# Kernel optimization log

Measured on AMD Instinct MI355X. Metric: run time of the kernel, lower is better.

Reference implementation:

```python
import jax, jax.numpy as jnp
import numpy as np

B, L, H2, P, A, T = 2048, 128, 600, 50, 50, 3  # batch, seq, 2*hidden, pos_emb, attn, latent types


def setup_inputs() -> dict:
    key = jax.random.key(0)
    ks = jax.random.split(key, 9)
    return {
        "hidden": jax.random.normal(ks[0], (B, L, H2), dtype=jnp.float32),
        "pos1_emb": jax.random.normal(ks[1], (B, L, P), dtype=jnp.float32),
        "pos2_emb": jax.random.normal(ks[2], (B, L, P), dtype=jnp.float32),
        "entity1_idx": jax.random.randint(ks[3], (B,), 0, L),
        "entity2_idx": jax.random.randint(ks[4], (B,), 0, L),
        "W_hid": jax.random.normal(ks[5], (A, H2 + 2 * P), dtype=jnp.float32) * 0.05,
        "W_ent": jax.random.normal(ks[6], (A, 4 * H2), dtype=jnp.float32) * 0.05,
        "latent_types": jax.random.normal(ks[7], (T, H2), dtype=jnp.float32) * 0.05,
        "v": jax.random.normal(ks[8], (A, 1), dtype=jnp.float32) * 0.05,
    }


def _latent_type(ent, latent_types):
    # ent: [B, 1, H2]; latent_types: [T, H2]
    a = jax.nn.softmax(jnp.einsum("bed,td->bet", ent, latent_types), axis=-1)
    return jnp.einsum("bet,td->bed", a, latent_types)  # [B, 1, H2]


def reference(hidden, pos1_emb, pos2_emb, entity1_idx, entity2_idx, W_hid, W_ent, latent_types, v):
    b = hidden.shape[0]
    batch_ix = jnp.arange(b)
    hid_e1 = hidden[batch_ix, entity1_idx][:, None, :]  # [B, 1, H2]
    hid_e2 = hidden[batch_ix, entity2_idx][:, None, :]
    e1_type = _latent_type(hid_e1, latent_types)
    e2_type = _latent_type(hid_e2, latent_types)
    # u1: per-token projection, u2: per-sentence entity projection (broadcast over L)
    u1 = jnp.einsum("bld,ad->bla", jnp.concatenate([hidden, pos1_emb, pos2_emb], axis=-1), W_hid)
    u2 = jnp.einsum("bed,ad->bea", jnp.concatenate([hid_e1, e1_type, hid_e2, e2_type], axis=-1), W_ent)
    u = jnp.tanh(u1 + u2)  # [B, L, A]
    scores = jnp.einsum("bla,a->bl", u, v[:, 0])  # [B, L]
    alpha = jax.nn.softmax(scores, axis=-1)
    z = jnp.einsum("bl,bld->bd", alpha, hidden)  # [B, H2]
    return z
```

## Files before the change

kernel.cpp:

```cpp
#include <hip/hip_runtime.h>
#include <hip/hip_bf16.h>
#include <math.h>


#define B_    2048
#define L_    128
#define H2_   600
#define P_    50
#define A_    50
#define D700  700
#define KCN   22
#define KHALF 11
#define AP    64
#define MT    32
#define XP    712
#define NB    8

typedef __attribute__((ext_vector_type(8))) short short8;
typedef __attribute__((ext_vector_type(4))) float f32x4;

__device__ __forceinline__ unsigned short f2bf(float f) {
  unsigned u = __float_as_uint(f);
  u += 0x7fffu + ((u >> 16) & 1u);
  return (unsigned short)(u >> 16);
}
__device__ __forceinline__ unsigned cvtpk(float a, float b) {
  unsigned r;
  asm("v_cvt_pk_bf16_f32 %0, %1, %2" : "=v"(r) : "v"(a), "v"(b));
  return r;
}
__device__ __forceinline__ float bf2f(unsigned short s) {
  return __uint_as_float(((unsigned)s) << 16);
}

__global__ __launch_bounds__(512, 4) void ku2(const float* __restrict__ hidden,
                                              const int* __restrict__ e1,
                                              const int* __restrict__ e2,
                                              const float* __restrict__ Went,
                                              const float* __restrict__ lt,
                                              const float* __restrict__ Wh,
                                              unsigned short* __restrict__ Wt,
                                              float* __restrict__ u2ws) {
  __shared__ __align__(16) float E[NB][2400];
  __shared__ float dots[NB][2][3];
  __shared__ float aw[NB][2][3];
  int tid = threadIdx.x;
  int b0 = blockIdx.x * NB;

  {
    int gidx = blockIdx.x * 512 + tid;
    if (gidx < KCN * 2048) {
      int kc = gidx >> 11, r = gidx & 2047, a = r >> 5, kk = r & 31;
      int d = kc * 32 + kk;
      float v = (a < A_ && d < D700) ? Wh[a * D700 + d] : 0.f;
      Wt[gidx] = f2bf(v);
    }
  }

  for (int idx = tid; idx < NB * 2 * 150; idx += 512) {
    int i = idx / 300, r = idx - i * 300, e = r / 150, g = r - e * 150;
    int bb = b0 + i;
    int l = e ? e2[bb] : e1[bb];
    float4 f = *(const float4*)(hidden + ((size_t)bb * L_ + l) * H2_ + g * 4);
    *(float4*)(&E[i][e * 1200 + g * 4]) = f;
  }
  __syncthreads();

  int w = tid >> 6, lane = tid & 63;
  #pragma unroll
  for (int j = 0; j < 6; ++j) {
    int i = w, e = (j >= 3) ? 1 : 0, t = j % 3;
    float p = 0.f;
    for (int d = lane; d < 600; d += 64) p += E[i][e * 1200 + d] * lt[t * 600 + d];
    #pragma unroll
    for (int mask = 1; mask <= 32; mask <<= 1) p += __shfl_xor(p, mask);
    if (lane == 0) dots[i][e][t] = p;
  }
  __syncthreads();
  if (tid < NB * 6) {
    int t = tid % 3, e = (tid / 3) & 1, i = tid / 6;
    float d0 = dots[i][e][0], d1 = dots[i][e][1], d2 = dots[i][e][2];
    float m = fmaxf(d0, fmaxf(d1, d2));
    float x0 = expf(d0 - m), x1 = expf(d1 - m), x2 = expf(d2 - m);
    float Z = x0 + x1 + x2;
    aw[i][e][t] = ((t == 0) ? x0 : (t == 1) ? x1 : x2) / Z;
  }
  __syncthreads();
  for (int idx = tid; idx < NB * 2 * 600; idx += 512) {
    int i = idx / 1200, r = idx - i * 1200, e = r / 600, d = r - e * 600;
    float v = aw[i][e][0] * lt[d] + aw[i][e][1] * lt[600 + d] + aw[i][e][2] * lt[1200 + d];
    E[i][e * 1200 + 600 + d] = v;
  }
  __syncthreads();
  for (int a = w; a < A_; a += 8) {
    float acc[NB] = {0.f, 0.f, 0.f, 0.f, 0.f, 0.f, 0.f, 0.f};
    for (int d0 = lane * 4; d0 < 2400; d0 += 256) {
      float4 wv = *(const float4*)(Went + a * 2400 + d0);
      #pragma unroll
      for (int i = 0; i < NB; ++i) {
        float4 ev = *(const float4*)(&E[i][d0]);
        acc[i] += ev.x * wv.x + ev.y * wv.y + ev.z * wv.z + ev.w * wv.w;
      }
    }
    #pragma unroll
    for (int i = 0; i < NB; ++i) {
      float p = acc[i];
      #pragma unroll
      for (int mask = 1; mask <= 32; mask <<= 1) p += __shfl_xor(p, mask);
      if (lane == 0) u2ws[(b0 + i) * AP + a] = p;
    }
  }
  for (int idx = tid; idx < NB * (AP - A_); idx += 512) {
    u2ws[(b0 + idx / (AP - A_)) * AP + A_ + idx % (AP - A_)] = 0.f;
  }
}

__global__ __launch_bounds__(512, 4) void kmain(
    const float* __restrict__ hidden, const float* __restrict__ pos1,
    const float* __restrict__ pos2, const float* __restrict__ vvec,
    const unsigned short* __restrict__ Wt, const float* __restrict__ u2ws,
    float* __restrict__ zp_ws, float* __restrict__ mS_ws) {
  __shared__ __align__(16) unsigned short Xs[MT * XP];
  __shared__ __align__(16) float pacc[4][64][8];
  __shared__ float scores4[4][MT];
  __shared__ float es_s[MT];
  __shared__ float u2s[AP];
  __shared__ float vs[AP];

  int tid = threadIdx.x;
  int T = blockIdx.x;
  int b = T >> 2, tok0 = (T & 3) * MT;
  int w = tid >> 6, lane = tid & 63;
  int acol = lane & 15, kgrp = lane >> 4;

  int t = tid >> 4, c0 = tid & 15;
  const float* rowp = hidden + ((size_t)(b * L_ + tok0) + t) * H2_;
  float4 f[9];
  #pragma unroll
  for (int j = 0; j < 9; ++j) f[j] = *(const float4*)(rowp + (c0 + 16 * j) * 4);
  bool h10 = (c0 < 6);
  float4 f9;
  if (h10) f9 = *(const float4*)(rowp + (c0 + 144) * 4);

  const float* p1 = pos1 + (size_t)(b * L_ + tok0) * P_;
  const float* p2 = pos2 + (size_t)(b * L_ + tok0) * P_;
  float2 q1a = *(const float2*)(p1 + tid * 2);
  float2 q2a = *(const float2*)(p2 + tid * 2);
  bool hq = (tid < 288);
  float2 q1b, q2b;
  if (hq) {
    q1b = *(const float2*)(p1 + (tid + 512) * 2);
    q2b = *(const float2*)(p2 + (tid + 512) * 2);
  }
  float u2v = 0.f, vvv = 0.f;
  if (tid < AP) {
    u2v = u2ws[b * AP + tid];
    vvv = (tid < A_) ? vvec[tid] : 0.f;
  }

  #pragma unroll
  for (int j = 0; j < 9; ++j) {
    uint2 wv2; wv2.x = cvtpk(f[j].x, f[j].y); wv2.y = cvtpk(f[j].z, f[j].w);
    *(uint2*)(&Xs[t * XP + (c0 + 16 * j) * 4]) = wv2;
  }
  if (h10) {
    uint2 wv2; wv2.x = cvtpk(f9.x, f9.y); wv2.y = cvtpk(f9.z, f9.w);
    *(uint2*)(&Xs[t * XP + (c0 + 144) * 4]) = wv2;
  }
  {
    int t1 = tid / 25, g = tid - t1 * 25;
    *(unsigned*)(&Xs[t1 * XP + 600 + g * 2]) = cvtpk(q1a.x, q1a.y);
    *(unsigned*)(&Xs[t1 * XP + 650 + g * 2]) = cvtpk(q2a.x, q2a.y);
  }
  if (hq) {
    int idx = tid + 512;
    int t1 = idx / 25, g = idx - t1 * 25;
    *(unsigned*)(&Xs[t1 * XP + 600 + g * 2]) = cvtpk(q1b.x, q1b.y);
    *(unsigned*)(&Xs[t1 * XP + 650 + g * 2]) = cvtpk(q2b.x, q2b.y);
  }
  if (tid < MT) {
    uint2 zz; zz.x = 0u; zz.y = 0u;
    *(uint2*)(&Xs[tid * XP + 700]) = zz;
  }
  if (tid < AP) { u2s[tid] = u2v; vs[tid] = vvv; }

  int at = w & 3;
  int kc0 = (w >> 2) * KHALF;
  const unsigned short* wbase = Wt + (at * 16 + acol) * 32 + kgrp * 8;
  short8 wf[KHALF];
  #pragma unroll
  for (int kc = 0; kc < KHALF; ++kc)
    wf[kc] = *(const short8*)(wbase + (kc0 + kc) * 2048);
  __syncthreads();

  f32x4 acc0 = {0.f, 0.f, 0.f, 0.f}, acc1 = {0.f, 0.f, 0.f, 0.f};
  #pragma unroll
  for (int kc = 0; kc < KHALF; ++kc) {
    int ke = (kc0 + kc) * 32 + kgrp * 8;
    short8 a0 = *(const short8*)(&Xs[acol * XP + ke]);
    short8 a1 = *(const short8*)(&Xs[(16 + acol) * XP + ke]);
    acc0 = __builtin_amdgcn_mfma_f32_16x16x32_bf16(a0, wf[kc], acc0, 0, 0, 0);
    acc1 = __builtin_amdgcn_mfma_f32_16x16x32_bf16(a1, wf[kc], acc1, 0, 0, 0);
  }

  if (w >= 4) {
    float4 pv0 = {acc0[0], acc0[1], acc0[2], acc0[3]};
    float4 pv1 = {acc1[0], acc1[1], acc1[2], acc1[3]};
    *(float4*)(&pacc[w - 4][lane][0]) = pv0;
    *(float4*)(&pacc[w - 4][lane][4]) = pv1;
  }
  __syncthreads();
  if (w < 4) {
    float va = vs[w * 16 + acol];
    float u2a = u2s[w * 16 + acol];
    float4 pv0 = *(const float4*)(&pacc[w][lane][0]);
    float4 pv1 = *(const float4*)(&pacc[w][lane][4]);
    float s0[4], s1[4];
    s0[0] = va * tanhf(acc0[0] + pv0.x + u2a);
    s0[1] = va * tanhf(acc0[1] + pv0.y + u2a);
    s0[2] = va * tanhf(acc0[2] + pv0.z + u2a);
    s0[3] = va * tanhf(acc0[3] + pv0.w + u2a);
    s1[0] = va * tanhf(acc1[0] + pv1.x + u2a);
    s1[1] = va * tanhf(acc1[1] + pv1.y + u2a);
    s1[2] = va * tanhf(acc1[2] + pv1.z + u2a);
    s1[3] = va * tanhf(acc1[3] + pv1.w + u2a);
    #pragma unroll
    for (int mask = 1; mask < 16; mask <<= 1) {
      #pragma unroll
      for (int r = 0; r < 4; ++r) {
        s0[r] += __shfl_xor(s0[r], mask);
        s1[r] += __shfl_xor(s1[r], mask);
      }
    }
    if (acol == 0) {
      #pragma unroll
      for (int r = 0; r < 4; ++r) {
        scores4[w][kgrp * 4 + r] = s0[r];
        scores4[w][16 + kgrp * 4 + r] = s1[r];
      }
    }
  }
  __syncthreads();

  if (tid < 64) {
    float s = (tid < MT)
                  ? (scores4[0][tid] + scores4[1][tid] + scores4[2][tid] + scores4[3][tid])
                  : -3.402823466e38f;
    float m = s;
    #pragma unroll
    for (int mask = 1; mask <= 32; mask <<= 1) m = fmaxf(m, __shfl_xor(m, mask));
    float e = (tid < MT) ? expf(s - m) : 0.f;
    float S = e;
    #pragma unroll
    for (int mask = 1; mask <= 32; mask <<= 1) S += __shfl_xor(S, mask);
    if (tid < MT) es_s[tid] = e;
    if (tid == 0) { mS_ws[T * 2] = m; mS_ws[T * 2 + 1] = S; }
  }
  __syncthreads();

  if (tid < 150) {
    float z0 = 0.f, z1 = 0.f, z2 = 0.f, z3 = 0.f;
    #pragma unroll
    for (int r = 0; r < MT; ++r) {
      uint2 xv = *(const uint2*)(&Xs[r * XP + tid * 4]);
      float e = es_s[r];
      z0 += e * bf2f((unsigned short)(xv.x & 0xffff));
      z1 += e * bf2f((unsigned short)(xv.x >> 16));
      z2 += e * bf2f((unsigned short)(xv.y & 0xffff));
      z3 += e * bf2f((unsigned short)(xv.y >> 16));
    }
    float4 wv = {z0, z1, z2, z3};
    *(float4*)(zp_ws + (size_t)T * 600 + tid * 4) = wv;
  }
}

__global__ __launch_bounds__(128) void kcomb(const float* __restrict__ zp_ws,
                                             const float* __restrict__ mS_ws,
                                             float* __restrict__ out) {
  int b = blockIdx.x, tid = threadIdx.x;
  float mq[4], Sq[4];
  #pragma unroll
  for (int qq = 0; qq < 4; ++qq) {
    mq[qq] = mS_ws[(b * 4 + qq) * 2];
    Sq[qq] = mS_ws[(b * 4 + qq) * 2 + 1];
  }
  float M = fmaxf(fmaxf(mq[0], mq[1]), fmaxf(mq[2], mq[3]));
  float c[4], Z = 0.f;
  #pragma unroll
  for (int qq = 0; qq < 4; ++qq) { c[qq] = expf(mq[qq] - M); Z += Sq[qq] * c[qq]; }
  float inv = 1.f / Z;
  for (int d = tid; d < 600; d += 128) {
    float z = 0.f;
    #pragma unroll
    for (int qq = 0; qq < 4; ++qq) z += c[qq] * zp_ws[(size_t)(b * 4 + qq) * 600 + d];
    out[b * 600 + d] = z * inv;
  }
}

extern "C" void kernel_launch(void* const* d_in, const int* in_sizes, int n_in,
                              void* d_out, int out_size, void* d_ws, size_t ws_size,
                              hipStream_t stream) {
  const float* hidden = (const float*)d_in[0];
  const float* pos1   = (const float*)d_in[1];
  const float* pos2   = (const float*)d_in[2];
  const int*   e1     = (const int*)d_in[3];
  const int*   e2     = (const int*)d_in[4];
  const float* Whid   = (const float*)d_in[5];
  const float* Went   = (const float*)d_in[6];
  const float* lt     = (const float*)d_in[7];
  const float* vvec   = (const float*)d_in[8];
  float* out = (float*)d_out;

  char* ws = (char*)d_ws;
  unsigned short* Wt = (unsigned short*)ws;
  float* u2ws  = (float*)(ws + 98304);
  float* mS_ws = (float*)(ws + 98304 + 524288);
  float* zp_ws = (float*)(ws + 98304 + 524288 + 131072);

  hipLaunchKernelGGL(ku2, dim3(B_ / NB), dim3(512), 0, stream, hidden, e1, e2, Went, lt,
                     Whid, Wt, u2ws);
  hipLaunchKernelGGL(kmain, dim3(B_ * 4), dim3(512), 0, stream, hidden, pos1, pos2, vvec,
                     Wt, u2ws, zp_ws, mS_ws);
  hipLaunchKernelGGL(kcomb, dim3(B_), dim3(128), 0, stream, zp_ws, mS_ws, out);
}
```

Before: 224.0 us.

## Make kmain persistent with double-buffered LDS prefetch of next tile

Turns the main attention kernel into a persistent kernel of 256 blocks, each walking 32 tiles with a stride of 256. The next tile's hidden and position rows are loaded into registers while the current tile runs its MFMA, tanh, softmax and weighted-sum stages, then written into a second LDS buffer. The bf16 weight fragments and v values are loaded once per block instead of once per tile. The cost is double the LDS footprint, lower occupancy (launch bounds 2), and only 256 blocks to spread over the GPU's CUs.

```diff
diff --git a/kernel.cpp b/kernel.cpp
--- a/kernel.cpp
+++ b/kernel.cpp
@@ -15,6 +15,8 @@
 #define MT    32
 #define XP    712
 #define NB    8
+#define GRIDM 256
+#define NTILE (B_ * 4)
 
 typedef __attribute__((ext_vector_type(8))) short short8;
 typedef __attribute__((ext_vector_type(4))) float f32x4;
@@ -115,162 +117,211 @@
   }
 }
 
-__global__ __launch_bounds__(512, 4) void kmain(
+__global__ __launch_bounds__(512, 2) void kmain(
     const float* __restrict__ hidden, const float* __restrict__ pos1,
     const float* __restrict__ pos2, const float* __restrict__ vvec,
     const unsigned short* __restrict__ Wt, const float* __restrict__ u2ws,
     float* __restrict__ zp_ws, float* __restrict__ mS_ws) {
-  __shared__ __align__(16) unsigned short Xs[MT * XP];
+  __shared__ __align__(16) unsigned short Xs[2][MT * XP];
   __shared__ __align__(16) float pacc[4][64][8];
   __shared__ float scores4[4][MT];
   __shared__ float es_s[MT];
-  __shared__ float u2s[AP];
-  __shared__ float vs[AP];
 
   int tid = threadIdx.x;
-  int T = blockIdx.x;
-  int b = T >> 2, tok0 = (T & 3) * MT;
   int w = tid >> 6, lane = tid & 63;
   int acol = lane & 15, kgrp = lane >> 4;
-
+  int at = w & 3, kc0 = (w >> 2) * KHALF;
+  int aidx = at * 16 + acol;
   int t = tid >> 4, c0 = tid & 15;
-  const float* rowp = hidden + ((size_t)(b * L_ + tok0) + t) * H2_;
-  float4 f[9];
-  #pragma unroll
-  for (int j = 0; j < 9; ++j) f[j] = *(const float4*)(rowp + (c0 + 16 * j) * 4);
   bool h10 = (c0 < 6);
-  float4 f9;
-  if (h10) f9 = *(const float4*)(rowp + (c0 + 144) * 4);
-
-  const float* p1 = pos1 + (size_t)(b * L_ + tok0) * P_;
-  const float* p2 = pos2 + (size_t)(b * L_ + tok0) * P_;
-  float2 q1a = *(const float2*)(p1 + tid * 2);
-  float2 q2a = *(const float2*)(p2 + tid * 2);
   bool hq = (tid < 288);
-  float2 q1b, q2b;
-  if (hq) {
-    q1b = *(const float2*)(p1 + (tid + 512) * 2);
-    q2b = *(const float2*)(p2 + (tid + 512) * 2);
-  }
-  float u2v = 0.f, vvv = 0.f;
-  if (tid < AP) {
-    u2v = u2ws[b * AP + tid];
-    vvv = (tid < A_) ? vvec[tid] : 0.f;
-  }
-
-  #pragma unroll
-  for (int j = 0; j < 9; ++j) {
-    uint2 wv2; wv2.x = cvtpk(f[j].x, f[j].y); wv2.y = cvtpk(f[j].z, f[j].w);
-    *(uint2*)(&Xs[t * XP + (c0 + 16 * j) * 4]) = wv2;
-  }
-  if (h10) {
-    uint2 wv2; wv2.x = cvtpk(f9.x, f9.y); wv2.y = cvtpk(f9.z, f9.w);
-    *(uint2*)(&Xs[t * XP + (c0 + 144) * 4]) = wv2;
-  }
-  {
-    int t1 = tid / 25, g = tid - t1 * 25;
-    *(unsigned*)(&Xs[t1 * XP + 600 + g * 2]) = cvtpk(q1a.x, q1a.y);
-    *(unsigned*)(&Xs[t1 * XP + 650 + g * 2]) = cvtpk(q2a.x, q2a.y);
-  }
-  if (hq) {
-    int idx = tid + 512;
-    int t1 = idx / 25, g = idx - t1 * 25;
-    *(unsigned*)(&Xs[t1 * XP + 600 + g * 2]) = cvtpk(q1b.x, q1b.y);
-    *(unsigned*)(&Xs[t1 * XP + 650 + g * 2]) = cvtpk(q2b.x, q2b.y);
-  }
-  if (tid < MT) {
-    uint2 zz; zz.x = 0u; zz.y = 0u;
-    *(uint2*)(&Xs[tid * XP + 700]) = zz;
-  }
-  if (tid < AP) { u2s[tid] = u2v; vs[tid] = vvv; }
-
-  int at = w & 3;
-  int kc0 = (w >> 2) * KHALF;
-  const unsigned short* wbase = Wt + (at * 16 + acol) * 32 + kgrp * 8;
+
+  const unsigned short* wbase = Wt + aidx * 32 + kgrp * 8;
   short8 wf[KHALF];
   #pragma unroll
   for (int kc = 0; kc < KHALF; ++kc)
     wf[kc] = *(const short8*)(wbase + (kc0 + kc) * 2048);
-  __syncthreads();
-
-  f32x4 acc0 = {0.f, 0.f, 0.f, 0.f}, acc1 = {0.f, 0.f, 0.f, 0.f};
-  #pragma unroll
-  for (int kc = 0; kc < KHALF; ++kc) {
-    int ke = (kc0 + kc) * 32 + kgrp * 8;
-    short8 a0 = *(const short8*)(&Xs[acol * XP + ke]);
-    short8 a1 = *(const short8*)(&Xs[(16 + acol) * XP + ke]);
-    acc0 = __builtin_amdgcn_mfma_f32_16x16x32_bf16(a0, wf[kc], acc0, 0, 0, 0);
-    acc1 = __builtin_amdgcn_mfma_f32_16x16x32_bf16(a1, wf[kc], acc1, 0, 0, 0);
-  }
-
-  if (w >= 4) {
-    float4 pv0 = {acc0[0], acc0[1], acc0[2], acc0[3]};
-    float4 pv1 = {acc1[0], acc1[1], acc1[2], acc1[3]};
-    *(float4*)(&pacc[w - 4][lane][0]) = pv0;
-    *(float4*)(&pacc[w - 4][lane][4]) = pv1;
-  }
-  __syncthreads();
-  if (w < 4) {
-    float va = vs[w * 16 + acol];
-    float u2a = u2s[w * 16 + acol];
-    float4 pv0 = *(const float4*)(&pacc[w][lane][0]);
-    float4 pv1 = *(const float4*)(&pacc[w][lane][4]);
-    float s0[4], s1[4];
-    s0[0] = va * tanhf(acc0[0] + pv0.x + u2a);
-    s0[1] = va * tanhf(acc0[1] + pv0.y + u2a);
-    s0[2] = va * tanhf(acc0[2] + pv0.z + u2a);
-    s0[3] = va * tanhf(acc0[3] + pv0.w + u2a);
-    s1[0] = va * tanhf(acc1[0] + pv1.x + u2a);
-    s1[1] = va * tanhf(acc1[1] + pv1.y + u2a);
-    s1[2] = va * tanhf(acc1[2] + pv1.z + u2a);
-    s1[3] = va * tanhf(acc1[3] + pv1.w + u2a);
-    #pragma unroll
-    for (int mask = 1; mask < 16; mask <<= 1) {
-      #pragma unroll
-      for (int r = 0; r < 4; ++r) {
-        s0[r] += __shfl_xor(s0[r], mask);
-        s1[r] += __shfl_xor(s1[r], mask);
-      }
-    }
-    if (acol == 0) {
-      #pragma unroll
-      for (int r = 0; r < 4; ++r) {
-        scores4[w][kgrp * 4 + r] = s0[r];
-        scores4[w][16 + kgrp * 4 + r] = s1[r];
-      }
-    }
-  }
-  __syncthreads();
+  float va = (aidx < A_) ? vvec[aidx] : 0.f;
 
   if (tid < 64) {
-    float s = (tid < MT)
-                  ? (scores4[0][tid] + scores4[1][tid] + scores4[2][tid] + scores4[3][tid])
-                  : -3.402823466e38f;
-    float m = s;
-    #pragma unroll
-    for (int mask = 1; mask <= 32; mask <<= 1) m = fmaxf(m, __shfl_xor(m, mask));
-    float e = (tid < MT) ? expf(s - m) : 0.f;
-    float S = e;
-    #pragma unroll
-    for (int mask = 1; mask <= 32; mask <<= 1) S += __shfl_xor(S, mask);
-    if (tid < MT) es_s[tid] = e;
-    if (tid == 0) { mS_ws[T * 2] = m; mS_ws[T * 2 + 1] = S; }
-  }
-  __syncthreads();
-
-  if (tid < 150) {
-    float z0 = 0.f, z1 = 0.f, z2 = 0.f, z3 = 0.f;
-    #pragma unroll
-    for (int r = 0; r < MT; ++r) {
-      uint2 xv = *(const uint2*)(&Xs[r * XP + tid * 4]);
-      float e = es_s[r];
-      z0 += e * bf2f((unsigned short)(xv.x & 0xffff));
-      z1 += e * bf2f((unsigned short)(xv.x >> 16));
-      z2 += e * bf2f((unsigned short)(xv.y & 0xffff));
-      z3 += e * bf2f((unsigned short)(xv.y >> 16));
-    }
-    float4 wv = {z0, z1, z2, z3};
-    *(float4*)(zp_ws + (size_t)T * 600 + tid * 4) = wv;
+    int hh = tid >> 5, row = tid & 31;
+    uint2 zz; zz.x = 0u; zz.y = 0u;
+    *(uint2*)(&Xs[hh][row * XP + 700]) = zz;
+  }
+
+  int T = blockIdx.x;
+  float u2cur;
+  {
+    int b = T >> 2, tok0 = (T & 3) * MT;
+    const float* rowp = hidden + ((size_t)(b * L_ + tok0) + t) * H2_;
+    float4 f[9];
+    #pragma unroll
+    for (int j = 0; j < 9; ++j) f[j] = *(const float4*)(rowp + (c0 + 16 * j) * 4);
+    float4 f9 = {0.f, 0.f, 0.f, 0.f};
+    if (h10) f9 = *(const float4*)(rowp + (c0 + 144) * 4);
+    const float* p1 = pos1 + (size_t)(b * L_ + tok0) * P_;
+    const float* p2 = pos2 + (size_t)(b * L_ + tok0) * P_;
+    float2 q1a = *(const float2*)(p1 + tid * 2);
+    float2 q2a = *(const float2*)(p2 + tid * 2);
+    float2 q1b = {0.f, 0.f}, q2b = {0.f, 0.f};
+    if (hq) {
+      q1b = *(const float2*)(p1 + (tid + 512) * 2);
+      q2b = *(const float2*)(p2 + (tid + 512) * 2);
+    }
+    u2cur = u2ws[b * AP + aidx];
+    #pragma unroll
+    for (int j = 0; j < 9; ++j) {
+      uint2 wv2; wv2.x = cvtpk(f[j].x, f[j].y); wv2.y = cvtpk(f[j].z, f[j].w);
+      *(uint2*)(&Xs[0][t * XP + (c0 + 16 * j) * 4]) = wv2;
+    }
+    if (h10) {
+      uint2 wv2; wv2.x = cvtpk(f9.x, f9.y); wv2.y = cvtpk(f9.z, f9.w);
+      *(uint2*)(&Xs[0][t * XP + (c0 + 144) * 4]) = wv2;
+    }
+    {
+      int t1 = tid / 25, g = tid - t1 * 25;
+      *(unsigned*)(&Xs[0][t1 * XP + 600 + g * 2]) = cvtpk(q1a.x, q1a.y);
+      *(unsigned*)(&Xs[0][t1 * XP + 650 + g * 2]) = cvtpk(q2a.x, q2a.y);
+    }
+    if (hq) {
+      int idx = tid + 512;
+      int t1 = idx / 25, g = idx - t1 * 25;
+      *(unsigned*)(&Xs[0][t1 * XP + 600 + g * 2]) = cvtpk(q1b.x, q1b.y);
+      *(unsigned*)(&Xs[0][t1 * XP + 650 + g * 2]) = cvtpk(q2b.x, q2b.y);
+    }
+  }
+  __syncthreads();
+
+  int cur = 0;
+  for (int k = 0; k < NTILE / GRIDM; ++k) {
+    bool hasnext = (k < NTILE / GRIDM - 1);
+    int Tn = T + GRIDM;
+
+    float4 f[9], f9 = {0.f, 0.f, 0.f, 0.f};
+    float2 q1a = {0.f, 0.f}, q2a = {0.f, 0.f}, q1b = {0.f, 0.f}, q2b = {0.f, 0.f};
+    float u2n = 0.f;
+    if (hasnext) {
+      int bn = Tn >> 2, tokn = (Tn & 3) * MT;
+      const float* rowp = hidden + ((size_t)(bn * L_ + tokn) + t) * H2_;
+      #pragma unroll
+      for (int j = 0; j < 9; ++j) f[j] = *(const float4*)(rowp + (c0 + 16 * j) * 4);
+      if (h10) f9 = *(const float4*)(rowp + (c0 + 144) * 4);
+      const float* p1 = pos1 + (size_t)(bn * L_ + tokn) * P_;
+      const float* p2 = pos2 + (size_t)(bn * L_ + tokn) * P_;
+      q1a = *(const float2*)(p1 + tid * 2);
+      q2a = *(const float2*)(p2 + tid * 2);
+      if (hq) {
+        q1b = *(const float2*)(p1 + (tid + 512) * 2);
+        q2b = *(const float2*)(p2 + (tid + 512) * 2);
+      }
+      u2n = u2ws[bn * AP + aidx];
+    }
+
+    f32x4 acc0 = {0.f, 0.f, 0.f, 0.f}, acc1 = {0.f, 0.f, 0.f, 0.f};
+    #pragma unroll
+    for (int kc = 0; kc < KHALF; ++kc) {
+      int ke = (kc0 + kc) * 32 + kgrp * 8;
+      short8 a0 = *(const short8*)(&Xs[cur][acol * XP + ke]);
+      short8 a1 = *(const short8*)(&Xs[cur][(16 + acol) * XP + ke]);
+      acc0 = __builtin_amdgcn_mfma_f32_16x16x32_bf16(a0, wf[kc], acc0, 0, 0, 0);
+      acc1 = __builtin_amdgcn_mfma_f32_16x16x32_bf16(a1, wf[kc], acc1, 0, 0, 0);
+    }
+
+    if (w >= 4) {
+      float4 pv0 = {acc0[0], acc0[1], acc0[2], acc0[3]};
+      float4 pv1 = {acc1[0], acc1[1], acc1[2], acc1[3]};
+      *(float4*)(&pacc[w - 4][lane][0]) = pv0;
+      *(float4*)(&pacc[w - 4][lane][4]) = pv1;
+    }
+    __syncthreads();
+    if (w < 4) {
+      float4 pv0 = *(const float4*)(&pacc[w][lane][0]);
+      float4 pv1 = *(const float4*)(&pacc[w][lane][4]);
+      float s0[4], s1[4];
+      s0[0] = va * tanhf(acc0[0] + pv0.x + u2cur);
+      s0[1] = va * tanhf(acc0[1] + pv0.y + u2cur);
+      s0[2] = va * tanhf(acc0[2] + pv0.z + u2cur);
+      s0[3] = va * tanhf(acc0[3] + pv0.w + u2cur);
+      s1[0] = va * tanhf(acc1[0] + pv1.x + u2cur);
+      s1[1] = va * tanhf(acc1[1] + pv1.y + u2cur);
+      s1[2] = va * tanhf(acc1[2] + pv1.z + u2cur);
+      s1[3] = va * tanhf(acc1[3] + pv1.w + u2cur);
+      #pragma unroll
+      for (int mask = 1; mask < 16; mask <<= 1) {
+        #pragma unroll
+        for (int r = 0; r < 4; ++r) {
+          s0[r] += __shfl_xor(s0[r], mask);
+          s1[r] += __shfl_xor(s1[r], mask);
+        }
+      }
+      if (acol == 0) {
+        #pragma unroll
+        for (int r = 0; r < 4; ++r) {
+          scores4[w][kgrp * 4 + r] = s0[r];
+          scores4[w][16 + kgrp * 4 + r] = s1[r];
+        }
+      }
+    }
+    __syncthreads();
+
+    if (tid < 64) {
+      float s = (tid < MT)
+                    ? (scores4[0][tid] + scores4[1][tid] + scores4[2][tid] + scores4[3][tid])
+                    : -3.402823466e38f;
+      float m = s;
+      #pragma unroll
+      for (int mask = 1; mask <= 32; mask <<= 1) m = fmaxf(m, __shfl_xor(m, mask));
+      float e = (tid < MT) ? expf(s - m) : 0.f;
+      float S = e;
+      #pragma unroll
+      for (int mask = 1; mask <= 32; mask <<= 1) S += __shfl_xor(S, mask);
+      if (tid < MT) es_s[tid] = e;
+      if (tid == 0) { mS_ws[T * 2] = m; mS_ws[T * 2 + 1] = S; }
+    }
+    __syncthreads();
+
+    if (tid < 150) {
+      float z0 = 0.f, z1 = 0.f, z2 = 0.f, z3 = 0.f;
+      #pragma unroll
+      for (int r = 0; r < MT; ++r) {
+        uint2 xv = *(const uint2*)(&Xs[cur][r * XP + tid * 4]);
+        float e = es_s[r];
+        z0 += e * bf2f((unsigned short)(xv.x & 0xffff));
+        z1 += e * bf2f((unsigned short)(xv.x >> 16));
+        z2 += e * bf2f((unsigned short)(xv.y & 0xffff));
+        z3 += e * bf2f((unsigned short)(xv.y >> 16));
+      }
+      float4 wv = {z0, z1, z2, z3};
+      *(float4*)(zp_ws + (size_t)T * 600 + tid * 4) = wv;
+    }
+
+    if (hasnext) {
+      unsigned short* Xn = &Xs[cur ^ 1][0];
+      #pragma unroll
+      for (int j = 0; j < 9; ++j) {
+        uint2 wv2; wv2.x = cvtpk(f[j].x, f[j].y); wv2.y = cvtpk(f[j].z, f[j].w);
+        *(uint2*)(&Xn[t * XP + (c0 + 16 * j) * 4]) = wv2;
+      }
+      if (h10) {
+        uint2 wv2; wv2.x = cvtpk(f9.x, f9.y); wv2.y = cvtpk(f9.z, f9.w);
+        *(uint2*)(&Xn[t * XP + (c0 + 144) * 4]) = wv2;
+      }
+      {
+        int t1 = tid / 25, g = tid - t1 * 25;
+        *(unsigned*)(&Xn[t1 * XP + 600 + g * 2]) = cvtpk(q1a.x, q1a.y);
+        *(unsigned*)(&Xn[t1 * XP + 650 + g * 2]) = cvtpk(q2a.x, q2a.y);
+      }
+      if (hq) {
+        int idx = tid + 512;
+        int t1 = idx / 25, g = idx - t1 * 25;
+        *(unsigned*)(&Xn[t1 * XP + 600 + g * 2]) = cvtpk(q1b.x, q1b.y);
+        *(unsigned*)(&Xn[t1 * XP + 650 + g * 2]) = cvtpk(q2b.x, q2b.y);
+      }
+    }
+    __syncthreads();
+    u2cur = u2n;
+    T = Tn;
+    cur ^= 1;
   }
 }
 
@@ -319,7 +370,7 @@
 
   hipLaunchKernelGGL(ku2, dim3(B_ / NB), dim3(512), 0, stream, hidden, e1, e2, Went, lt,
                      Whid, Wt, u2ws);
-  hipLaunchKernelGGL(kmain, dim3(B_ * 4), dim3(512), 0, stream, hidden, pos1, pos2, vvec,
+  hipLaunchKernelGGL(kmain, dim3(GRIDM), dim3(512), 0, stream, hidden, pos1, pos2, vvec,
                      Wt, u2ws, zp_ws, mS_ws);
   hipLaunchKernelGGL(kcomb, dim3(B_), dim3(128), 0, stream, zp_ws, mS_ws, out);
 }
```

After: 242.3 us. 8.2% more time.

## Raise occupancy by cutting LDS and registers in main attention kernel

Applied to the files above, without the earlier changes.

Launch bounds go from 4 to 6 blocks per CU. To fit, the cross-wave partial-accumulator buffer is stored as bf16 instead of fp32, and the u2/v shared arrays are dropped in favour of per-lane global loads. The hidden-row loads are split into two phases so fewer float4 registers are live at once. The aim is more resident waves to hide global-load latency, at the cost of extra rounding in the partial MFMA sums and possible register spills under the tighter register budget.

```diff
diff --git a/kernel.cpp b/kernel.cpp
--- a/kernel.cpp
+++ b/kernel.cpp
@@ -115,78 +115,82 @@
   }
 }
 
-__global__ __launch_bounds__(512, 4) void kmain(
+__global__ __launch_bounds__(512, 6) void kmain(
     const float* __restrict__ hidden, const float* __restrict__ pos1,
     const float* __restrict__ pos2, const float* __restrict__ vvec,
     const unsigned short* __restrict__ Wt, const float* __restrict__ u2ws,
     float* __restrict__ zp_ws, float* __restrict__ mS_ws) {
   __shared__ __align__(16) unsigned short Xs[MT * XP];
-  __shared__ __align__(16) float pacc[4][64][8];
+  __shared__ __align__(16) unsigned short pacc[4][64][8];
   __shared__ float scores4[4][MT];
   __shared__ float es_s[MT];
-  __shared__ float u2s[AP];
-  __shared__ float vs[AP];
 
   int tid = threadIdx.x;
   int T = blockIdx.x;
   int b = T >> 2, tok0 = (T & 3) * MT;
   int w = tid >> 6, lane = tid & 63;
   int acol = lane & 15, kgrp = lane >> 4;
+  int at = w & 3, kc0 = (w >> 2) * KHALF;
+  int aidx = at * 16 + acol;
+
+  float u2v = u2ws[b * AP + aidx];
+  float va = (aidx < A_) ? vvec[aidx] : 0.f;
 
   int t = tid >> 4, c0 = tid & 15;
   const float* rowp = hidden + ((size_t)(b * L_ + tok0) + t) * H2_;
-  float4 f[9];
-  #pragma unroll
-  for (int j = 0; j < 9; ++j) f[j] = *(const float4*)(rowp + (c0 + 16 * j) * 4);
-  bool h10 = (c0 < 6);
-  float4 f9;
-  if (h10) f9 = *(const float4*)(rowp + (c0 + 144) * 4);
-
-  const float* p1 = pos1 + (size_t)(b * L_ + tok0) * P_;
-  const float* p2 = pos2 + (size_t)(b * L_ + tok0) * P_;
-  float2 q1a = *(const float2*)(p1 + tid * 2);
-  float2 q2a = *(const float2*)(p2 + tid * 2);
-  bool hq = (tid < 288);
-  float2 q1b, q2b;
-  if (hq) {
-    q1b = *(const float2*)(p1 + (tid + 512) * 2);
-    q2b = *(const float2*)(p2 + (tid + 512) * 2);
-  }
-  float u2v = 0.f, vvv = 0.f;
-  if (tid < AP) {
-    u2v = u2ws[b * AP + tid];
-    vvv = (tid < A_) ? vvec[tid] : 0.f;
-  }
-
-  #pragma unroll
-  for (int j = 0; j < 9; ++j) {
-    uint2 wv2; wv2.x = cvtpk(f[j].x, f[j].y); wv2.y = cvtpk(f[j].z, f[j].w);
-    *(uint2*)(&Xs[t * XP + (c0 + 16 * j) * 4]) = wv2;
-  }
-  if (h10) {
-    uint2 wv2; wv2.x = cvtpk(f9.x, f9.y); wv2.y = cvtpk(f9.z, f9.w);
-    *(uint2*)(&Xs[t * XP + (c0 + 144) * 4]) = wv2;
-  }
   {
-    int t1 = tid / 25, g = tid - t1 * 25;
-    *(unsigned*)(&Xs[t1 * XP + 600 + g * 2]) = cvtpk(q1a.x, q1a.y);
-    *(unsigned*)(&Xs[t1 * XP + 650 + g * 2]) = cvtpk(q2a.x, q2a.y);
-  }
-  if (hq) {
-    int idx = tid + 512;
-    int t1 = idx / 25, g = idx - t1 * 25;
-    *(unsigned*)(&Xs[t1 * XP + 600 + g * 2]) = cvtpk(q1b.x, q1b.y);
-    *(unsigned*)(&Xs[t1 * XP + 650 + g * 2]) = cvtpk(q2b.x, q2b.y);
+    float4 f[5];
+    #pragma unroll
+    for (int j = 0; j < 5; ++j) f[j] = *(const float4*)(rowp + (c0 + 16 * j) * 4);
+    #pragma unroll
+    for (int j = 0; j < 5; ++j) {
+      uint2 wv2; wv2.x = cvtpk(f[j].x, f[j].y); wv2.y = cvtpk(f[j].z, f[j].w);
+      *(uint2*)(&Xs[t * XP + (c0 + 16 * j) * 4]) = wv2;
+    }
+  }
+  {
+    bool h10 = (c0 < 6);
+    float4 f[4], f9 = {0.f, 0.f, 0.f, 0.f};
+    #pragma unroll
+    for (int j = 0; j < 4; ++j) f[j] = *(const float4*)(rowp + (c0 + 16 * (5 + j)) * 4);
+    if (h10) f9 = *(const float4*)(rowp + (c0 + 144) * 4);
+    const float* p1 = pos1 + (size_t)(b * L_ + tok0) * P_;
+    const float* p2 = pos2 + (size_t)(b * L_ + tok0) * P_;
+    float2 q1a = *(const float2*)(p1 + tid * 2);
+    float2 q2a = *(const float2*)(p2 + tid * 2);
+    bool hq = (tid < 288);
+    float2 q1b = {0.f, 0.f}, q2b = {0.f, 0.f};
+    if (hq) {
+      q1b = *(const float2*)(p1 + (tid + 512) * 2);
+      q2b = *(const float2*)(p2 + (tid + 512) * 2);
+    }
+    #pragma unroll
+    for (int j = 0; j < 4; ++j) {
+      uint2 wv2; wv2.x = cvtpk(f[j].x, f[j].y); wv2.y = cvtpk(f[j].z, f[j].w);
+      *(uint2*)(&Xs[t * XP + (c0 + 16 * (5 + j)) * 4]) = wv2;
+    }
+    if (h10) {
+      uint2 wv2; wv2.x = cvtpk(f9.x, f9.y); wv2.y = cvtpk(f9.z, f9.w);
+      *(uint2*)(&Xs[t * XP + (c0 + 144) * 4]) = wv2;
+    }
+    {
+      int t1 = tid / 25, g = tid - t1 * 25;
+      *(unsigned*)(&Xs[t1 * XP + 600 + g * 2]) = cvtpk(q1a.x, q1a.y);
+      *(unsigned*)(&Xs[t1 * XP + 650 + g * 2]) = cvtpk(q2a.x, q2a.y);
+    }
+    if (hq) {
+      int idx = tid + 512;
+      int t1 = idx / 25, g = idx - t1 * 25;
+      *(unsigned*)(&Xs[t1 * XP + 600 + g * 2]) = cvtpk(q1b.x, q1b.y);
+      *(unsigned*)(&Xs[t1 * XP + 650 + g * 2]) = cvtpk(q2b.x, q2b.y);
+    }
   }
   if (tid < MT) {
     uint2 zz; zz.x = 0u; zz.y = 0u;
     *(uint2*)(&Xs[tid * XP + 700]) = zz;
   }
-  if (tid < AP) { u2s[tid] = u2v; vs[tid] = vvv; }
-
-  int at = w & 3;
-  int kc0 = (w >> 2) * KHALF;
-  const unsigned short* wbase = Wt + (at * 16 + acol) * 32 + kgrp * 8;
+
+  const unsigned short* wbase = Wt + aidx * 32 + kgrp * 8;
   short8 wf[KHALF];
   #pragma unroll
   for (int kc = 0; kc < KHALF; ++kc)
@@ -204,26 +208,29 @@
   }
 
   if (w >= 4) {
-    float4 pv0 = {acc0[0], acc0[1], acc0[2], acc0[3]};
-    float4 pv1 = {acc1[0], acc1[1], acc1[2], acc1[3]};
-    *(float4*)(&pacc[w - 4][lane][0]) = pv0;
-    *(float4*)(&pacc[w - 4][lane][4]) = pv1;
+    uint4 pk;
+    pk.x = cvtpk(acc0[0], acc0[1]);
+    pk.y = cvtpk(acc0[2], acc0[3]);
+    pk.z = cvtpk(acc1[0], acc1[1]);
+    pk.w = cvtpk(acc1[2], acc1[3]);
+    *(uint4*)(&pacc[w - 4][lane][0]) = pk;
   }
   __syncthreads();
   if (w < 4) {
-    float va = vs[w * 16 + acol];
-    float u2a = u2s[w * 16 + acol];
-    float4 pv0 = *(const float4*)(&pacc[w][lane][0]);
-    float4 pv1 = *(const float4*)(&pacc[w][lane][4]);
+    uint4 pk = *(const uint4*)(&pacc[w][lane][0]);
+    float pv0x = bf2f((unsigned short)(pk.x & 0xffff)), pv0y = bf2f((unsigned short)(pk.x >> 16));
+    float pv0z = bf2f((unsigned short)(pk.y & 0xffff)), pv0w = bf2f((unsigned short)(pk.y >> 16));
+    float pv1x = bf2f((unsigned short)(pk.z & 0xffff)), pv1y = bf2f((unsigned short)(pk.z >> 16));
+    float pv1z = bf2f((unsigned short)(pk.w & 0xffff)), pv1w = bf2f((unsigned short)(pk.w >> 16));
     float s0[4], s1[4];
-    s0[0] = va * tanhf(acc0[0] + pv0.x + u2a);
-    s0[1] = va * tanhf(acc0[1] + pv0.y + u2a);
-    s0[2] = va * tanhf(acc0[2] + pv0.z + u2a);
-    s0[3] = va * tanhf(acc0[3] + pv0.w + u2a);
-    s1[0] = va * tanhf(acc1[0] + pv1.x + u2a);
-    s1[1] = va * tanhf(acc1[1] + pv1.y + u2a);
-    s1[2] = va * tanhf(acc1[2] + pv1.z + u2a);
-    s1[3] = va * tanhf(acc1[3] + pv1.w + u2a);
+    s0[0] = va * tanhf(acc0[0] + pv0x + u2v);
+    s0[1] = va * tanhf(acc0[1] + pv0y + u2v);
+    s0[2] = va * tanhf(acc0[2] + pv0z + u2v);
+    s0[3] = va * tanhf(acc0[3] + pv0w + u2v);
+    s1[0] = va * tanhf(acc1[0] + pv1x + u2v);
+    s1[1] = va * tanhf(acc1[1] + pv1y + u2v);
+    s1[2] = va * tanhf(acc1[2] + pv1z + u2v);
+    s1[3] = va * tanhf(acc1[3] + pv1w + u2v);
     #pragma unroll
     for (int mask = 1; mask < 16; mask <<= 1) {
       #pragma unroll
```

After: 227.4 us. No clear change (+1.5%).

## Process whole sentence per block with prefetched chunks and fused softmax combine

Applied to the files above, without the earlier changes.

Each block now handles all 128 tokens of one batch row in four 32-token chunks, instead of one chunk per block. It prefetches the next chunk's hidden and position rows into registers while the MFMA for the current chunk runs. The online-softmax combine is done in-block, which removes the partial-result workspace writes and the separate kcomb kernel launch. Weight fragments are loaded once per batch row instead of once per chunk. The cost is fewer blocks (2048 instead of 8192), more registers per thread for the prefetch buffers, and extra barriers per chunk, which could lower occupancy and the latency hiding it provides.

```diff
diff --git a/kernel.cpp b/kernel.cpp
--- a/kernel.cpp
+++ b/kernel.cpp
@@ -119,181 +119,219 @@
     const float* __restrict__ hidden, const float* __restrict__ pos1,
     const float* __restrict__ pos2, const float* __restrict__ vvec,
     const unsigned short* __restrict__ Wt, const float* __restrict__ u2ws,
-    float* __restrict__ zp_ws, float* __restrict__ mS_ws) {
+    float* __restrict__ out) {
   __shared__ __align__(16) unsigned short Xs[MT * XP];
   __shared__ __align__(16) float pacc[4][64][8];
   __shared__ float scores4[4][MT];
   __shared__ float es_s[MT];
-  __shared__ float u2s[AP];
-  __shared__ float vs[AP];
+  __shared__ float msl[4][2];
 
   int tid = threadIdx.x;
-  int T = blockIdx.x;
-  int b = T >> 2, tok0 = (T & 3) * MT;
+  int b = blockIdx.x;
   int w = tid >> 6, lane = tid & 63;
   int acol = lane & 15, kgrp = lane >> 4;
-
+  int at = w & 3, kc0 = (w >> 2) * KHALF;
+  int aidx = at * 16 + acol;
   int t = tid >> 4, c0 = tid & 15;
-  const float* rowp = hidden + ((size_t)(b * L_ + tok0) + t) * H2_;
-  float4 f[9];
+  bool h10 = (c0 < 6);
+  bool hq = (tid < 288);
+
+  float u2v = u2ws[b * AP + aidx];
+  float va = (aidx < A_) ? vvec[aidx] : 0.f;
+  const unsigned short* wbase = Wt + aidx * 32 + kgrp * 8;
+  const float* hb = hidden + (size_t)b * L_ * H2_;
+  const float* p1b = pos1 + (size_t)b * L_ * P_;
+  const float* p2b = pos2 + (size_t)b * L_ * P_;
+
+  float4 zacc[4];
   #pragma unroll
-  for (int j = 0; j < 9; ++j) f[j] = *(const float4*)(rowp + (c0 + 16 * j) * 4);
-  bool h10 = (c0 < 6);
-  float4 f9;
-  if (h10) f9 = *(const float4*)(rowp + (c0 + 144) * 4);
-
-  const float* p1 = pos1 + (size_t)(b * L_ + tok0) * P_;
-  const float* p2 = pos2 + (size_t)(b * L_ + tok0) * P_;
-  float2 q1a = *(const float2*)(p1 + tid * 2);
-  float2 q2a = *(const float2*)(p2 + tid * 2);
-  bool hq = (tid < 288);
-  float2 q1b, q2b;
-  if (hq) {
-    q1b = *(const float2*)(p1 + (tid + 512) * 2);
-    q2b = *(const float2*)(p2 + (tid + 512) * 2);
-  }
-  float u2v = 0.f, vvv = 0.f;
-  if (tid < AP) {
-    u2v = u2ws[b * AP + tid];
-    vvv = (tid < A_) ? vvec[tid] : 0.f;
-  }
-
-  #pragma unroll
-  for (int j = 0; j < 9; ++j) {
-    uint2 wv2; wv2.x = cvtpk(f[j].x, f[j].y); wv2.y = cvtpk(f[j].z, f[j].w);
-    *(uint2*)(&Xs[t * XP + (c0 + 16 * j) * 4]) = wv2;
-  }
-  if (h10) {
-    uint2 wv2; wv2.x = cvtpk(f9.x, f9.y); wv2.y = cvtpk(f9.z, f9.w);
-    *(uint2*)(&Xs[t * XP + (c0 + 144) * 4]) = wv2;
-  }
+  for (int q = 0; q < 4; ++q) { zacc[q].x = 0.f; zacc[q].y = 0.f; zacc[q].z = 0.f; zacc[q].w = 0.f; }
+
   {
-    int t1 = tid / 25, g = tid - t1 * 25;
-    *(unsigned*)(&Xs[t1 * XP + 600 + g * 2]) = cvtpk(q1a.x, q1a.y);
-    *(unsigned*)(&Xs[t1 * XP + 650 + g * 2]) = cvtpk(q2a.x, q2a.y);
-  }
-  if (hq) {
-    int idx = tid + 512;
-    int t1 = idx / 25, g = idx - t1 * 25;
-    *(unsigned*)(&Xs[t1 * XP + 600 + g * 2]) = cvtpk(q1b.x, q1b.y);
-    *(unsigned*)(&Xs[t1 * XP + 650 + g * 2]) = cvtpk(q2b.x, q2b.y);
-  }
-  if (tid < MT) {
-    uint2 zz; zz.x = 0u; zz.y = 0u;
-    *(uint2*)(&Xs[tid * XP + 700]) = zz;
-  }
-  if (tid < AP) { u2s[tid] = u2v; vs[tid] = vvv; }
-
-  int at = w & 3;
-  int kc0 = (w >> 2) * KHALF;
-  const unsigned short* wbase = Wt + (at * 16 + acol) * 32 + kgrp * 8;
+    const float* rowp = hb + (size_t)t * H2_;
+    float4 f[9], f9 = {0.f, 0.f, 0.f, 0.f};
+    #pragma unroll
+    for (int j = 0; j < 9; ++j) f[j] = *(const float4*)(rowp + (c0 + 16 * j) * 4);
+    if (h10) f9 = *(const float4*)(rowp + (c0 + 144) * 4);
+    float2 q1a = *(const float2*)(p1b + tid * 2);
+    float2 q2a = *(const float2*)(p2b + tid * 2);
+    float2 q1b = {0.f, 0.f}, q2b = {0.f, 0.f};
+    if (hq) {
+      q1b = *(const float2*)(p1b + (tid + 512) * 2);
+      q2b = *(const float2*)(p2b + (tid + 512) * 2);
+    }
+    #pragma unroll
+    for (int j = 0; j < 9; ++j) {
+      uint2 wv2; wv2.x = cvtpk(f[j].x, f[j].y); wv2.y = cvtpk(f[j].z, f[j].w);
+      *(uint2*)(&Xs[t * XP + (c0 + 16 * j) * 4]) = wv2;
+    }
+    if (h10) {
+      uint2 wv2; wv2.x = cvtpk(f9.x, f9.y); wv2.y = cvtpk(f9.z, f9.w);
+      *(uint2*)(&Xs[t * XP + (c0 + 144) * 4]) = wv2;
+    }
+    {
+      int t1 = tid / 25, g = tid - t1 * 25;
+      *(unsigned*)(&Xs[t1 * XP + 600 + g * 2]) = cvtpk(q1a.x, q1a.y);
+      *(unsigned*)(&Xs[t1 * XP + 650 + g * 2]) = cvtpk(q2a.x, q2a.y);
+    }
+    if (hq) {
+      int idx = tid + 512;
+      int t1 = idx / 25, g = idx - t1 * 25;
+      *(unsigned*)(&Xs[t1 * XP + 600 + g * 2]) = cvtpk(q1b.x, q1b.y);
+      *(unsigned*)(&Xs[t1 * XP + 650 + g * 2]) = cvtpk(q2b.x, q2b.y);
+    }
+    if (tid < MT) {
+      uint2 zz; zz.x = 0u; zz.y = 0u;
+      *(uint2*)(&Xs[tid * XP + 700]) = zz;
+    }
+  }
   short8 wf[KHALF];
   #pragma unroll
   for (int kc = 0; kc < KHALF; ++kc)
     wf[kc] = *(const short8*)(wbase + (kc0 + kc) * 2048);
   __syncthreads();
 
-  f32x4 acc0 = {0.f, 0.f, 0.f, 0.f}, acc1 = {0.f, 0.f, 0.f, 0.f};
   #pragma unroll
-  for (int kc = 0; kc < KHALF; ++kc) {
-    int ke = (kc0 + kc) * 32 + kgrp * 8;
-    short8 a0 = *(const short8*)(&Xs[acol * XP + ke]);
-    short8 a1 = *(const short8*)(&Xs[(16 + acol) * XP + ke]);
-    acc0 = __builtin_amdgcn_mfma_f32_16x16x32_bf16(a0, wf[kc], acc0, 0, 0, 0);
-    acc1 = __builtin_amdgcn_mfma_f32_16x16x32_bf16(a1, wf[kc], acc1, 0, 0, 0);
-  }
-
-  if (w >= 4) {
-    float4 pv0 = {acc0[0], acc0[1], acc0[2], acc0[3]};
-    float4 pv1 = {acc1[0], acc1[1], acc1[2], acc1[3]};
-    *(float4*)(&pacc[w - 4][lane][0]) = pv0;
-    *(float4*)(&pacc[w - 4][lane][4]) = pv1;
-  }
-  __syncthreads();
-  if (w < 4) {
-    float va = vs[w * 16 + acol];
-    float u2a = u2s[w * 16 + acol];
-    float4 pv0 = *(const float4*)(&pacc[w][lane][0]);
-    float4 pv1 = *(const float4*)(&pacc[w][lane][4]);
-    float s0[4], s1[4];
-    s0[0] = va * tanhf(acc0[0] + pv0.x + u2a);
-    s0[1] = va * tanhf(acc0[1] + pv0.y + u2a);
-    s0[2] = va * tanhf(acc0[2] + pv0.z + u2a);
-    s0[3] = va * tanhf(acc0[3] + pv0.w + u2a);
-    s1[0] = va * tanhf(acc1[0] + pv1.x + u2a);
-    s1[1] = va * tanhf(acc1[1] + pv1.y + u2a);
-    s1[2] = va * tanhf(acc1[2] + pv1.z + u2a);
-    s1[3] = va * tanhf(acc1[3] + pv1.w + u2a);
-    #pragma unroll
-    for (int mask = 1; mask < 16; mask <<= 1) {
-      #pragma unroll
-      for (int r = 0; r < 4; ++r) {
-        s0[r] += __shfl_xor(s0[r], mask);
-        s1[r] += __shfl_xor(s1[r], mask);
-      }
-    }
-    if (acol == 0) {
-      #pragma unroll
-      for (int r = 0; r < 4; ++r) {
-        scores4[w][kgrp * 4 + r] = s0[r];
-        scores4[w][16 + kgrp * 4 + r] = s1[r];
-      }
-    }
-  }
-  __syncthreads();
-
-  if (tid < 64) {
-    float s = (tid < MT)
-                  ? (scores4[0][tid] + scores4[1][tid] + scores4[2][tid] + scores4[3][tid])
-                  : -3.402823466e38f;
-    float m = s;
-    #pragma unroll
-    for (int mask = 1; mask <= 32; mask <<= 1) m = fmaxf(m, __shfl_xor(m, mask));
-    float e = (tid < MT) ? expf(s - m) : 0.f;
-    float S = e;
-    #pragma unroll
-    for (int mask = 1; mask <= 32; mask <<= 1) S += __shfl_xor(S, mask);
-    if (tid < MT) es_s[tid] = e;
-    if (tid == 0) { mS_ws[T * 2] = m; mS_ws[T * 2 + 1] = S; }
-  }
-  __syncthreads();
+  for (int q = 0; q < 4; ++q) {
+    bool hasnext = (q < 3);
+    const float* rowpn = hb + ((size_t)((q + 1) * MT) + t) * H2_;
+
+    float4 nf[9]; float4 nf9 = {0.f, 0.f, 0.f, 0.f};
+    float2 nq1a = {0.f, 0.f}, nq2a = {0.f, 0.f}, nq1b = {0.f, 0.f}, nq2b = {0.f, 0.f};
+    if (hasnext) {
+      #pragma unroll
+      for (int j = 0; j < 5; ++j) nf[j] = *(const float4*)(rowpn + (c0 + 16 * j) * 4);
+    }
+
+    f32x4 acc0 = {0.f, 0.f, 0.f, 0.f}, acc1 = {0.f, 0.f, 0.f, 0.f};
+    #pragma unroll
+    for (int kc = 0; kc < KHALF; ++kc) {
+      int ke = (kc0 + kc) * 32 + kgrp * 8;
+      short8 a0 = *(const short8*)(&Xs[acol * XP + ke]);
+      short8 a1 = *(const short8*)(&Xs[(16 + acol) * XP + ke]);
+      acc0 = __builtin_amdgcn_mfma_f32_16x16x32_bf16(a0, wf[kc], acc0, 0, 0, 0);
+      acc1 = __builtin_amdgcn_mfma_f32_16x16x32_bf16(a1, wf[kc], acc1, 0, 0, 0);
+    }
+
+    if (hasnext) {
+      #pragma unroll
+      for (int j = 5; j < 9; ++j) nf[j] = *(const float4*)(rowpn + (c0 + 16 * j) * 4);
+      if (h10) nf9 = *(const float4*)(rowpn + (c0 + 144) * 4);
+      const float* p1n = p1b + (q + 1) * MT * P_;
+      const float* p2n = p2b + (q + 1) * MT * P_;
+      nq1a = *(const float2*)(p1n + tid * 2);
+      nq2a = *(const float2*)(p2n + tid * 2);
+      if (hq) {
+        nq1b = *(const float2*)(p1n + (tid + 512) * 2);
+        nq2b = *(const float2*)(p2n + (tid + 512) * 2);
+      }
+    }
+
+    if (w >= 4) {
+      float4 pv0 = {acc0[0], acc0[1], acc0[2], acc0[3]};
+      float4 pv1 = {acc1[0], acc1[1], acc1[2], acc1[3]};
+      *(float4*)(&pacc[w - 4][lane][0]) = pv0;
+      *(float4*)(&pacc[w - 4][lane][4]) = pv1;
+    }
+    __syncthreads();
+    if (w < 4) {
+      float4 pv0 = *(const float4*)(&pacc[w][lane][0]);
+      float4 pv1 = *(const float4*)(&pacc[w][lane][4]);
+      float s0[4], s1[4];
+      s0[0] = va * tanhf(acc0[0] + pv0.x + u2v);
+      s0[1] = va * tanhf(acc0[1] + pv0.y + u2v);
+      s0[2] = va * tanhf(acc0[2] + pv0.z + u2v);
+      s0[3] = va * tanhf(acc0[3] + pv0.w + u2v);
+      s1[0] = va * tanhf(acc1[0] + pv1.x + u2v);
+      s1[1] = va * tanhf(acc1[1] + pv1.y + u2v);
+      s1[2] = va * tanhf(acc1[2] + pv1.z + u2v);
+      s1[3] = va * tanhf(acc1[3] + pv1.w + u2v);
+      #pragma unroll
+      for (int mask = 1; mask < 16; mask <<= 1) {
+        #pragma unroll
+        for (int r = 0; r < 4; ++r) {
+          s0[r] += __shfl_xor(s0[r], mask);
+          s1[r] += __shfl_xor(s1[r], mask);
+        }
+      }
+      if (acol == 0) {
+        #pragma unroll
+        for (int r = 0; r < 4; ++r) {
+          scores4[w][kgrp * 4 + r] = s0[r];
+          scores4[w][16 + kgrp * 4 + r] = s1[r];
+        }
+      }
+    }
+    __syncthreads();
+
+    if (tid < 64) {
+      float s = (tid < MT)
+                    ? (scores4[0][tid] + scores4[1][tid] + scores4[2][tid] + scores4[3][tid])
+                    : -3.402823466e38f;
+      float m = s;
+      #pragma unroll
+      for (int mask = 1; mask <= 32; mask <<= 1) m = fmaxf(m, __shfl_xor(m, mask));
+      float e = (tid < MT) ? expf(s - m) : 0.f;
+      float S = e;
+      #pragma unroll
+      for (int mask = 1; mask <= 32; mask <<= 1) S += __shfl_xor(S, mask);
+      if (tid < MT) es_s[tid] = e;
+      if (tid == 0) { msl[q][0] = m; msl[q][1] = S; }
+    }
+    __syncthreads();
+
+    if (tid < 150) {
+      float z0 = 0.f, z1 = 0.f, z2 = 0.f, z3 = 0.f;
+      #pragma unroll
+      for (int r = 0; r < MT; ++r) {
+        uint2 xv = *(const uint2*)(&Xs[r * XP + tid * 4]);
+        float e = es_s[r];
+        z0 += e * bf2f((unsigned short)(xv.x & 0xffff));
+        z1 += e * bf2f((unsigned short)(xv.x >> 16));
+        z2 += e * bf2f((unsigned short)(xv.y & 0xffff));
+        z3 += e * bf2f((unsigned short)(xv.y >> 16));
+      }
+      zacc[q].x = z0; zacc[q].y = z1; zacc[q].z = z2; zacc[q].w = z3;
+    }
+    __syncthreads();
+
+    if (hasnext) {
+      #pragma unroll
+      for (int j = 0; j < 9; ++j) {
+        uint2 wv2; wv2.x = cvtpk(nf[j].x, nf[j].y); wv2.y = cvtpk(nf[j].z, nf[j].w);
+        *(uint2*)(&Xs[t * XP + (c0 + 16 * j) * 4]) = wv2;
+      }
+      if (h10) {
+        uint2 wv2; wv2.x = cvtpk(nf9.x, nf9.y); wv2.y = cvtpk(nf9.z, nf9.w);
+        *(uint2*)(&Xs[t * XP + (c0 + 144) * 4]) = wv2;
+      }
+      {
+        int t1 = tid / 25, g = tid - t1 * 25;
+        *(unsigned*)(&Xs[t1 * XP + 600 + g * 2]) = cvtpk(nq1a.x, nq1a.y);
+        *(unsigned*)(&Xs[t1 * XP + 650 + g * 2]) = cvtpk(nq2a.x, nq2a.y);
+      }
+      if (hq) {
+        int idx = tid + 512;
+        int t1 = idx / 25, g = idx - t1 * 25;
+        *(unsigned*)(&Xs[t1 * XP + 600 + g * 2]) = cvtpk(nq1b.x, nq1b.y);
+        *(unsigned*)(&Xs[t1 * XP + 650 + g * 2]) = cvtpk(nq2b.x, nq2b.y);
+      }
+      __syncthreads();
+    }
+  }
 
   if (tid < 150) {
-    float z0 = 0.f, z1 = 0.f, z2 = 0.f, z3 = 0.f;
-    #pragma unroll
-    for (int r = 0; r < MT; ++r) {
-      uint2 xv = *(const uint2*)(&Xs[r * XP + tid * 4]);
-      float e = es_s[r];
-      z0 += e * bf2f((unsigned short)(xv.x & 0xffff));
-      z1 += e * bf2f((unsigned short)(xv.x >> 16));
-      z2 += e * bf2f((unsigned short)(xv.y & 0xffff));
-      z3 += e * bf2f((unsigned short)(xv.y >> 16));
-    }
-    float4 wv = {z0, z1, z2, z3};
-    *(float4*)(zp_ws + (size_t)T * 600 + tid * 4) = wv;
-  }
-}
-
-__global__ __launch_bounds__(128) void kcomb(const float* __restrict__ zp_ws,
-                                             const float* __restrict__ mS_ws,
-                                             float* __restrict__ out) {
-  int b = blockIdx.x, tid = threadIdx.x;
-  float mq[4], Sq[4];
-  #pragma unroll
-  for (int qq = 0; qq < 4; ++qq) {
-    mq[qq] = mS_ws[(b * 4 + qq) * 2];
-    Sq[qq] = mS_ws[(b * 4 + qq) * 2 + 1];
-  }
-  float M = fmaxf(fmaxf(mq[0], mq[1]), fmaxf(mq[2], mq[3]));
-  float c[4], Z = 0.f;
-  #pragma unroll
-  for (int qq = 0; qq < 4; ++qq) { c[qq] = expf(mq[qq] - M); Z += Sq[qq] * c[qq]; }
-  float inv = 1.f / Z;
-  for (int d = tid; d < 600; d += 128) {
-    float z = 0.f;
-    #pragma unroll
-    for (int qq = 0; qq < 4; ++qq) z += c[qq] * zp_ws[(size_t)(b * 4 + qq) * 600 + d];
-    out[b * 600 + d] = z * inv;
+    float m0 = msl[0][0], m1 = msl[1][0], m2 = msl[2][0], m3 = msl[3][0];
+    float M = fmaxf(fmaxf(m0, m1), fmaxf(m2, m3));
+    float c0_ = expf(m0 - M), c1_ = expf(m1 - M), c2_ = expf(m2 - M), c3_ = expf(m3 - M);
+    float Z = msl[0][1] * c0_ + msl[1][1] * c1_ + msl[2][1] * c2_ + msl[3][1] * c3_;
+    float inv = 1.f / Z;
+    float4 r;
+    r.x = (zacc[0].x * c0_ + zacc[1].x * c1_ + zacc[2].x * c2_ + zacc[3].x * c3_) * inv;
+    r.y = (zacc[0].y * c0_ + zacc[1].y * c1_ + zacc[2].y * c2_ + zacc[3].y * c3_) * inv;
+    r.z = (zacc[0].z * c0_ + zacc[1].z * c1_ + zacc[2].z * c2_ + zacc[3].z * c3_) * inv;
+    r.w = (zacc[0].w * c0_ + zacc[1].w * c1_ + zacc[2].w * c2_ + zacc[3].w * c3_) * inv;
+    *(float4*)(out + (size_t)b * 600 + tid * 4) = r;
   }
 }
 
@@ -314,12 +352,9 @@
   char* ws = (char*)d_ws;
   unsigned short* Wt = (unsigned short*)ws;
   float* u2ws  = (float*)(ws + 98304);
-  float* mS_ws = (float*)(ws + 98304 + 524288);
-  float* zp_ws = (float*)(ws + 98304 + 524288 + 131072);
 
   hipLaunchKernelGGL(ku2, dim3(B_ / NB), dim3(512), 0, stream, hidden, e1, e2, Went, lt,
                      Whid, Wt, u2ws);
-  hipLaunchKernelGGL(kmain, dim3(B_ * 4), dim3(512), 0, stream, hidden, pos1, pos2, vvec,
-                     Wt, u2ws, zp_ws, mS_ws);
-  hipLaunchKernelGGL(kcomb, dim3(B_), dim3(128), 0, stream, zp_ws, mS_ws, out);
-}
+  hipLaunchKernelGGL(kmain, dim3(B_), dim3(512), 0, stream, hidden, pos1, pos2, vvec,
+                     Wt, u2ws, out);
+}
```

After: 349.4 us. +56.0%, slower.
